# Optimization experiments

Hardware: AMD Instinct MI355X
Metric: run time of the kernel (lower is better)

Reference implementation:

```python
import jax, jax.numpy as jnp
import numpy as np


def setup_inputs() -> dict:
    key = jax.random.key(0)
    x = jax.random.normal(key, (4096, 4096), dtype=jnp.float32)
    return {"x": x}


def reference(x):
    """IDCT (DCT-III) along the last axis, scaled by 2 as in DREAMPlace:
        out[k] = x[0] + 2 * sum_{n=1}^{N-1} x[n] * cos(pi*n*(2k+1)/(2N))
    computed via a 2N-point FFT with twiddle-factor (expk) pre-multiply.
    """
    N = x.shape[-1]
    # twiddle expk[n] = exp(j*pi*n/(2N))
    theta = (jnp.pi / (2.0 * N)) * jnp.arange(N, dtype=jnp.float32)
    expk = jax.lax.complex(jnp.cos(theta), jnp.sin(theta))  # complex64 [N]
    c = x.astype(jnp.complex64) * expk                       # [M, N]
    # zero-pad to 2N; S[k] = sum_n c[n] exp(+j*2*pi*n*k/(2N)) = conj(fft(conj(c2)))[k]
    c2 = jnp.concatenate([c, jnp.zeros_like(c)], axis=-1)    # [M, 2N]
    S = jnp.fft.fft(jnp.conj(c2))                            # Re(S) == Re(2N*ifft(c2))
    # out[k] = 2*Re(S[k]) - x[0]
    y = 2.0 * jnp.real(S[..., :N]) - x[..., :1]
    return y.astype(x.dtype)
```

## Files before the change

kernel.cpp:

```cpp
#include <hip/hip_runtime.h>
#include <stdint.h>


#define Md 4096
#define Nfull 4096
#define Ph 2048
#define Kh 2048
#define BM 128
#define BN 128
#define BK 64

typedef short bf16x8 __attribute__((ext_vector_type(8)));
typedef float floatx4 __attribute__((ext_vector_type(4)));
typedef unsigned short ushort_t;

__device__ __forceinline__ ushort_t f2bf(float f) {
  union { float f; uint32_t u; } v; v.f = f;
  uint32_t u = v.u;
  return (ushort_t)((u + 0x7fffu + ((u >> 16) & 1u)) >> 16);
}

__global__ __launch_bounds__(256) void prep_kernel(const float* __restrict__ x,
                                                   ushort_t* __restrict__ A,
                                                   ushort_t* __restrict__ Ce,
                                                   ushort_t* __restrict__ Co) {
  int b = blockIdx.x;
  if (b < 8192) {
    int i = (b * 256 + threadIdx.x) * 8;
    int m = i >> 12;
    int j = i & 4095;
    float4 a = *(const float4*)(x + i);
    float4 c = *(const float4*)(x + i + 4);
    union { ushort_t us[4]; int2 v; } ev, od;
    ev.us[0] = f2bf(a.x); od.us[0] = f2bf(a.y);
    ev.us[1] = f2bf(a.z); od.us[1] = f2bf(a.w);
    ev.us[2] = f2bf(c.x); od.us[2] = f2bf(c.y);
    ev.us[3] = f2bf(c.z); od.us[3] = f2bf(c.w);
    int half = j >> 1;
    *(int2*)(A + m * Nfull + half) = ev.v;
    *(int2*)(A + m * Nfull + Ph + half) = od.v;
  } else {
    int idx = ((b - 8192) * 256 + threadIdx.x) * 8;
    const float s = 3.14159265358979f / 8192.0f;
    union { ushort_t us[8]; int4 v; } pk;
    if (idx < Ph * Kh) {
      int p = idx >> 11;
      int ne0 = idx & 2047;
      int tp = 2 * p + 1;
#pragma unroll
      for (int jj = 0; jj < 8; ++jj) {
        int n = 2 * (ne0 + jj);
        int t = (n * tp) & 16383;
        float c = (n == 0) ? 1.0f : 2.0f * __cosf(s * (float)t);
        pk.us[jj] = f2bf(c);
      }
      *(int4*)(Ce + idx) = pk.v;
    } else {
      int local = idx - Ph * Kh;
      int p = local >> 11;
      int no0 = local & 2047;
      int tp = 2 * p + 1;
#pragma unroll
      for (int jj = 0; jj < 8; ++jj) {
        int n = 2 * (no0 + jj) + 1;
        int t = (n * tp) & 16383;
        pk.us[jj] = f2bf(2.0f * __cosf(s * (float)t));
      }
      *(int4*)(Co + local) = pk.v;
    }
  }
}

__global__ __launch_bounds__(256, 2) void gemm_fused(const ushort_t* __restrict__ A,
                                                     const ushort_t* __restrict__ Ce,
                                                     const ushort_t* __restrict__ Co,
                                                     float* __restrict__ out) {
  __shared__ __align__(16) ushort_t AsE[BM * BK];
  __shared__ __align__(16) ushort_t AsO[BM * BK];
  __shared__ __align__(16) ushort_t BsE[BN * BK];
  __shared__ __align__(16) ushort_t BsO[BN * BK];

  const int tid = threadIdx.x;
  const int wid = tid >> 6;
  const int lane = tid & 63;

  const int bm = blockIdx.y * BM;
  const int bn = blockIdx.x * BN;

  const int wm = (wid & 1) * 64;
  const int wn = (wid >> 1) * 64;

  const int lrow = lane & 15;
  const int kq = (lane >> 4) * 8;

  floatx4 accE[4][4] = {};
  floatx4 accO[4][4] = {};

  const int rr = tid >> 3;
  const int ee = (tid & 7) * 8;
  const int lb = wid * 512;

  const ushort_t* Ae = A + (size_t)bm * Nfull;
  const ushort_t* Ao = Ae + Ph;
  const ushort_t* Be = Ce + (size_t)bn * Kh;
  const ushort_t* Bo = Co + (size_t)bn * Kh;

#define GLDS(src, dst) __builtin_amdgcn_global_load_lds( \
      (const __attribute__((address_space(1))) void*)(src), \
      (__attribute__((address_space(3))) void*)(dst), 16, 0, 0)

  for (int k0 = 0; k0 < Kh; k0 += BK) {
#pragma unroll
    for (int i = 0; i < 4; ++i) {
      int r = i * 32 + rr;
      int l = i * 2048 + lb;
      GLDS(Ae + (size_t)r * Nfull + k0 + ee, AsE + l);
      GLDS(Ao + (size_t)r * Nfull + k0 + ee, AsO + l);
      GLDS(Be + (size_t)r * Kh   + k0 + ee, BsE + l);
      GLDS(Bo + (size_t)r * Kh   + k0 + ee, BsO + l);
    }
    __syncthreads();

#pragma unroll
    for (int kk = 0; kk < 2; ++kk) {
      const int ko = kk * 32 + kq;
      bf16x8 bE[4], bO[4];
#pragma unroll
      for (int f = 0; f < 4; ++f) {
        bE[f] = *(const bf16x8*)(BsE + (wn + f * 16 + lrow) * BK + ko);
        bO[f] = *(const bf16x8*)(BsO + (wn + f * 16 + lrow) * BK + ko);
      }
#pragma unroll
      for (int im = 0; im < 4; ++im) {
        bf16x8 aE = *(const bf16x8*)(AsE + (wm + im * 16 + lrow) * BK + ko);
        bf16x8 aO = *(const bf16x8*)(AsO + (wm + im * 16 + lrow) * BK + ko);
#pragma unroll
        for (int jn = 0; jn < 4; ++jn) {
          accE[im][jn] = __builtin_amdgcn_mfma_f32_16x16x32_bf16(aE, bE[jn], accE[im][jn], 0, 0, 0);
          accO[im][jn] = __builtin_amdgcn_mfma_f32_16x16x32_bf16(aO, bO[jn], accO[im][jn], 0, 0, 0);
        }
      }
    }
    __syncthreads();
  }
#undef GLDS

#pragma unroll
  for (int im = 0; im < 4; ++im) {
    int rb = bm + wm + im * 16 + (lane >> 4) * 4;
#pragma unroll
    for (int jn = 0; jn < 4; ++jn) {
      int p = bn + wn + jn * 16 + lrow;
      float* lo = out + (size_t)rb * Nfull + p;
      float* hi = out + (size_t)rb * Nfull + (Nfull - 1 - p);
#pragma unroll
      for (int r = 0; r < 4; ++r) {
        float e = accE[im][jn][r];
        float o = accO[im][jn][r];
        lo[(size_t)r * Nfull] = e + o;
        hi[(size_t)r * Nfull] = e - o;
      }
    }
  }
}

extern "C" void kernel_launch(void* const* d_in, const int* in_sizes, int n_in,
                              void* d_out, int out_size, void* d_ws, size_t ws_size,
                              hipStream_t stream) {
  const float* x = (const float*)d_in[0];
  float* out = (float*)d_out;
  ushort_t* Axb = (ushort_t*)d_ws;
  ushort_t* Ce = Axb + (size_t)Md * Nfull;
  ushort_t* Co = Ce + (size_t)Ph * Kh;

  prep_kernel<<<12288, 256, 0, stream>>>(x, Axb, Ce, Co);

  dim3 grid(Ph / BN, Md / BM);
  gemm_fused<<<grid, 256, 0, stream>>>(Axb, Ce, Co, out);
}
```

Baseline: 195.2 us.

## Swizzle LDS tile layout to fragment-major order and widen prep conversion stores

The GEMM's global-to-LDS copy now places data so each 16-row by 32-k MFMA fragment is contiguous. Each lane reads its 16-byte operand at lane*8, which removes the strided row-major LDS reads and their bank conflicts. The prep kernel handles 16 floats per thread with 16-byte stores for the even and odd halves, halving its block count. The global load pattern changes to 16 rows by 32 columns per wave chunk, which may reduce global coalescing width per row.

```diff
diff --git a/kernel.cpp b/kernel.cpp
--- a/kernel.cpp
+++ b/kernel.cpp
@@ -25,22 +25,30 @@
                                                    ushort_t* __restrict__ Ce,
                                                    ushort_t* __restrict__ Co) {
   int b = blockIdx.x;
-  if (b < 8192) {
-    int i = (b * 256 + threadIdx.x) * 8;
+  int tid = threadIdx.x;
+  if (b < 4096) {
+    int i = (b * 256 + tid) * 16;
     int m = i >> 12;
     int j = i & 4095;
-    float4 a = *(const float4*)(x + i);
-    float4 c = *(const float4*)(x + i + 4);
-    union { ushort_t us[4]; int2 v; } ev, od;
-    ev.us[0] = f2bf(a.x); od.us[0] = f2bf(a.y);
-    ev.us[1] = f2bf(a.z); od.us[1] = f2bf(a.w);
-    ev.us[2] = f2bf(c.x); od.us[2] = f2bf(c.y);
-    ev.us[3] = f2bf(c.z); od.us[3] = f2bf(c.w);
+    const float4* xp = (const float4*)(x + i);
+    float4 a0 = xp[0];
+    float4 a1 = xp[1];
+    float4 a2 = xp[2];
+    float4 a3 = xp[3];
+    union { ushort_t us[8]; int4 v; } ev, od;
+    ev.us[0] = f2bf(a0.x); od.us[0] = f2bf(a0.y);
+    ev.us[1] = f2bf(a0.z); od.us[1] = f2bf(a0.w);
+    ev.us[2] = f2bf(a1.x); od.us[2] = f2bf(a1.y);
+    ev.us[3] = f2bf(a1.z); od.us[3] = f2bf(a1.w);
+    ev.us[4] = f2bf(a2.x); od.us[4] = f2bf(a2.y);
+    ev.us[5] = f2bf(a2.z); od.us[5] = f2bf(a2.w);
+    ev.us[6] = f2bf(a3.x); od.us[6] = f2bf(a3.y);
+    ev.us[7] = f2bf(a3.z); od.us[7] = f2bf(a3.w);
     int half = j >> 1;
-    *(int2*)(A + m * Nfull + half) = ev.v;
-    *(int2*)(A + m * Nfull + Ph + half) = od.v;
+    *(int4*)(A + (size_t)m * Nfull + half) = ev.v;
+    *(int4*)(A + (size_t)m * Nfull + Ph + half) = od.v;
   } else {
-    int idx = ((b - 8192) * 256 + threadIdx.x) * 8;
+    int idx = ((b - 4096) * 256 + tid) * 8;
     const float s = 3.14159265358979f / 8192.0f;
     union { ushort_t us[8]; int4 v; } pk;
     if (idx < Ph * Kh) {
@@ -91,19 +99,21 @@
   const int wn = (wid >> 1) * 64;
 
   const int lrow = lane & 15;
-  const int kq = (lane >> 4) * 8;
 
   floatx4 accE[4][4] = {};
   floatx4 accO[4][4] = {};
 
-  const int rr = tid >> 3;
-  const int ee = (tid & 7) * 8;
+  const int srow = ((tid >> 7) << 4) | (tid & 15);
+  const int scol = ((tid >> 6) & 1) * 32 + ((tid >> 4) & 3) * 8;
   const int lb = wid * 512;
 
   const ushort_t* Ae = A + (size_t)bm * Nfull;
   const ushort_t* Ao = Ae + Ph;
   const ushort_t* Be = Ce + (size_t)bn * Kh;
   const ushort_t* Bo = Co + (size_t)bn * Kh;
+
+  const size_t aoff0 = (size_t)srow * Nfull + scol;
+  const size_t boff0 = (size_t)srow * Kh + scol;
 
 #define GLDS(src, dst) __builtin_amdgcn_global_load_lds( \
       (const __attribute__((address_space(1))) void*)(src), \
@@ -112,28 +122,30 @@
   for (int k0 = 0; k0 < Kh; k0 += BK) {
 #pragma unroll
     for (int i = 0; i < 4; ++i) {
-      int r = i * 32 + rr;
+      size_t ao = aoff0 + (size_t)(i * 32) * Nfull + k0;
+      size_t bo = boff0 + (size_t)(i * 32) * Kh + k0;
       int l = i * 2048 + lb;
-      GLDS(Ae + (size_t)r * Nfull + k0 + ee, AsE + l);
-      GLDS(Ao + (size_t)r * Nfull + k0 + ee, AsO + l);
-      GLDS(Be + (size_t)r * Kh   + k0 + ee, BsE + l);
-      GLDS(Bo + (size_t)r * Kh   + k0 + ee, BsO + l);
+      GLDS(Ae + ao, AsE + l);
+      GLDS(Ao + ao, AsO + l);
+      GLDS(Be + bo, BsE + l);
+      GLDS(Bo + bo, BsO + l);
     }
     __syncthreads();
 
 #pragma unroll
     for (int kk = 0; kk < 2; ++kk) {
-      const int ko = kk * 32 + kq;
       bf16x8 bE[4], bO[4];
 #pragma unroll
       for (int f = 0; f < 4; ++f) {
-        bE[f] = *(const bf16x8*)(BsE + (wn + f * 16 + lrow) * BK + ko);
-        bO[f] = *(const bf16x8*)(BsO + (wn + f * 16 + lrow) * BK + ko);
+        int off = ((wn >> 4) + f) * 1024 + kk * 512 + lane * 8;
+        bE[f] = *(const bf16x8*)(BsE + off);
+        bO[f] = *(const bf16x8*)(BsO + off);
       }
 #pragma unroll
       for (int im = 0; im < 4; ++im) {
-        bf16x8 aE = *(const bf16x8*)(AsE + (wm + im * 16 + lrow) * BK + ko);
-        bf16x8 aO = *(const bf16x8*)(AsO + (wm + im * 16 + lrow) * BK + ko);
+        int off = ((wm >> 4) + im) * 1024 + kk * 512 + lane * 8;
+        bf16x8 aE = *(const bf16x8*)(AsE + off);
+        bf16x8 aO = *(const bf16x8*)(AsO + off);
 #pragma unroll
         for (int jn = 0; jn < 4; ++jn) {
           accE[im][jn] = __builtin_amdgcn_mfma_f32_16x16x32_bf16(aE, bE[jn], accE[im][jn], 0, 0, 0);
@@ -173,7 +185,7 @@
   ushort_t* Ce = Axb + (size_t)Md * Nfull;
   ushort_t* Co = Ce + (size_t)Ph * Kh;
 
-  prep_kernel<<<12288, 256, 0, stream>>>(x, Axb, Ce, Co);
+  prep_kernel<<<8192, 256, 0, stream>>>(x, Axb, Ce, Co);
 
   dim3 grid(Ph / BN, Md / BM);
   gemm_fused<<<grid, 256, 0, stream>>>(Axb, Ce, Co, out);
```

Measured after the change: 236.9 us. 1.21x slower.

## Pre-tile operands into K-block layout and double-buffer LDS in GEMM

Applied to the files above, without the earlier changes.

The prep kernel now writes the even/odd input planes and the cosine tables into a tiled layout: 128-row by 32-k blocks, each stored contiguously in a k-group-major order. The GEMM then loads each stage with fully contiguous global_load_lds transfers into a double-buffered LDS region, issuing the next stage's loads before computing the current one. This halves BK to 32 and drops one barrier per iteration, aiming to overlap global loads with MFMA work and to make LDS fragment reads conflict-free. The cost is twice as many K iterations and a larger LDS footprint, which may limit occupancy.

```diff
diff --git a/kernel.cpp b/kernel.cpp
--- a/kernel.cpp
+++ b/kernel.cpp
@@ -8,7 +8,9 @@
 #define Kh 2048
 #define BM 128
 #define BN 128
-#define BK 64
+#define BK 32
+#define NKB 64
+#define TILE 4096
 
 typedef short bf16x8 __attribute__((ext_vector_type(8)));
 typedef float floatx4 __attribute__((ext_vector_type(4)));
@@ -21,136 +23,153 @@
 }
 
 __global__ __launch_bounds__(256) void prep_kernel(const float* __restrict__ x,
-                                                   ushort_t* __restrict__ A,
+                                                   ushort_t* __restrict__ Ae,
+                                                   ushort_t* __restrict__ Ao,
                                                    ushort_t* __restrict__ Ce,
                                                    ushort_t* __restrict__ Co) {
   int b = blockIdx.x;
-  if (b < 8192) {
-    int i = (b * 256 + threadIdx.x) * 8;
-    int m = i >> 12;
-    int j = i & 4095;
-    float4 a = *(const float4*)(x + i);
-    float4 c = *(const float4*)(x + i + 4);
-    union { ushort_t us[4]; int2 v; } ev, od;
-    ev.us[0] = f2bf(a.x); od.us[0] = f2bf(a.y);
-    ev.us[1] = f2bf(a.z); od.us[1] = f2bf(a.w);
-    ev.us[2] = f2bf(c.x); od.us[2] = f2bf(c.y);
-    ev.us[3] = f2bf(c.z); od.us[3] = f2bf(c.w);
-    int half = j >> 1;
-    *(int2*)(A + m * Nfull + half) = ev.v;
-    *(int2*)(A + m * Nfull + Ph + half) = od.v;
+  int t = threadIdx.x;
+  if (b < 2048) {
+    int bm = b >> 6, kb = b & 63;
+    int r = t >> 1, h = t & 1;
+    const float4* xp = (const float4*)(x + (((size_t)(bm * 128 + r)) << 12) + kb * 64 + h * 32);
+    float4 v0 = xp[0], v1 = xp[1], v2 = xp[2], v3 = xp[3];
+    float4 v4 = xp[4], v5 = xp[5], v6 = xp[6], v7 = xp[7];
+    union { ushort_t us[8]; int4 v; } e0, e1, o0, o1;
+    e0.us[0] = f2bf(v0.x); o0.us[0] = f2bf(v0.y);
+    e0.us[1] = f2bf(v0.z); o0.us[1] = f2bf(v0.w);
+    e0.us[2] = f2bf(v1.x); o0.us[2] = f2bf(v1.y);
+    e0.us[3] = f2bf(v1.z); o0.us[3] = f2bf(v1.w);
+    e0.us[4] = f2bf(v2.x); o0.us[4] = f2bf(v2.y);
+    e0.us[5] = f2bf(v2.z); o0.us[5] = f2bf(v2.w);
+    e0.us[6] = f2bf(v3.x); o0.us[6] = f2bf(v3.y);
+    e0.us[7] = f2bf(v3.z); o0.us[7] = f2bf(v3.w);
+    e1.us[0] = f2bf(v4.x); o1.us[0] = f2bf(v4.y);
+    e1.us[1] = f2bf(v4.z); o1.us[1] = f2bf(v4.w);
+    e1.us[2] = f2bf(v5.x); o1.us[2] = f2bf(v5.y);
+    e1.us[3] = f2bf(v5.z); o1.us[3] = f2bf(v5.w);
+    e1.us[4] = f2bf(v6.x); o1.us[4] = f2bf(v6.y);
+    e1.us[5] = f2bf(v6.z); o1.us[5] = f2bf(v6.w);
+    e1.us[6] = f2bf(v7.x); o1.us[6] = f2bf(v7.y);
+    e1.us[7] = f2bf(v7.z); o1.us[7] = f2bf(v7.w);
+    size_t tb = ((size_t)(bm * 64 + kb)) << 12;
+    int c0 = (2 * h) * 1024 + r * 8;
+    int c1 = c0 + 1024;
+    *(int4*)(Ae + tb + c0) = e0.v;
+    *(int4*)(Ae + tb + c1) = e1.v;
+    *(int4*)(Ao + tb + c0) = o0.v;
+    *(int4*)(Ao + tb + c1) = o1.v;
   } else {
-    int idx = ((b - 8192) * 256 + threadIdx.x) * 8;
+    int b2 = b - 2048;
+    int plane = b2 >> 10;
+    int bn = (b2 & 1023) >> 6, kb = b2 & 63;
+    ushort_t* T = plane ? Co : Ce;
+    size_t tb = ((size_t)(bn * 64 + kb)) << 12;
     const float s = 3.14159265358979f / 8192.0f;
-    union { ushort_t us[8]; int4 v; } pk;
-    if (idx < Ph * Kh) {
-      int p = idx >> 11;
-      int ne0 = idx & 2047;
+#pragma unroll
+    for (int half = 0; half < 2; ++half) {
+      int cc = t + half * 256;
+      int g = cc >> 7, r = cc & 127;
+      int p = bn * 128 + r;
       int tp = 2 * p + 1;
+      int ni = kb * 32 + g * 8;
+      union { ushort_t us[8]; int4 v; } pk;
 #pragma unroll
       for (int jj = 0; jj < 8; ++jj) {
-        int n = 2 * (ne0 + jj);
-        int t = (n * tp) & 16383;
-        float c = (n == 0) ? 1.0f : 2.0f * __cosf(s * (float)t);
+        int n = 2 * (ni + jj) + plane;
+        int ang = (n * tp) & 16383;
+        float c = (n == 0) ? 1.0f : 2.0f * __cosf(s * (float)ang);
         pk.us[jj] = f2bf(c);
       }
-      *(int4*)(Ce + idx) = pk.v;
-    } else {
-      int local = idx - Ph * Kh;
-      int p = local >> 11;
-      int no0 = local & 2047;
-      int tp = 2 * p + 1;
-#pragma unroll
-      for (int jj = 0; jj < 8; ++jj) {
-        int n = 2 * (no0 + jj) + 1;
-        int t = (n * tp) & 16383;
-        pk.us[jj] = f2bf(2.0f * __cosf(s * (float)t));
-      }
-      *(int4*)(Co + local) = pk.v;
+      *(int4*)(T + tb + cc * 8) = pk.v;
     }
   }
 }
 
-__global__ __launch_bounds__(256, 2) void gemm_fused(const ushort_t* __restrict__ A,
+__global__ __launch_bounds__(256, 2) void gemm_fused(const ushort_t* __restrict__ Ae,
+                                                     const ushort_t* __restrict__ Ao,
                                                      const ushort_t* __restrict__ Ce,
                                                      const ushort_t* __restrict__ Co,
                                                      float* __restrict__ out) {
-  __shared__ __align__(16) ushort_t AsE[BM * BK];
-  __shared__ __align__(16) ushort_t AsO[BM * BK];
-  __shared__ __align__(16) ushort_t BsE[BN * BK];
-  __shared__ __align__(16) ushort_t BsO[BN * BK];
+  __shared__ __align__(16) ushort_t S[32768];
 
   const int tid = threadIdx.x;
   const int wid = tid >> 6;
   const int lane = tid & 63;
 
-  const int bm = blockIdx.y * BM;
-  const int bn = blockIdx.x * BN;
+  const int bm = blockIdx.y;
+  const int bn = blockIdx.x;
 
   const int wm = (wid & 1) * 64;
   const int wn = (wid >> 1) * 64;
-
   const int lrow = lane & 15;
-  const int kq = (lane >> 4) * 8;
 
   floatx4 accE[4][4] = {};
   floatx4 accO[4][4] = {};
 
-  const int rr = tid >> 3;
-  const int ee = (tid & 7) * 8;
   const int lb = wid * 512;
-
-  const ushort_t* Ae = A + (size_t)bm * Nfull;
-  const ushort_t* Ao = Ae + Ph;
-  const ushort_t* Be = Ce + (size_t)bn * Kh;
-  const ushort_t* Bo = Co + (size_t)bn * Kh;
+  const ushort_t* pAe = Ae + (((size_t)bm * NKB) << 12) + (tid << 3);
+  const ushort_t* pAo = Ao + (((size_t)bm * NKB) << 12) + (tid << 3);
+  const ushort_t* pBe = Ce + (((size_t)bn * NKB) << 12) + (tid << 3);
+  const ushort_t* pBo = Co + (((size_t)bn * NKB) << 12) + (tid << 3);
 
 #define GLDS(src, dst) __builtin_amdgcn_global_load_lds( \
       (const __attribute__((address_space(1))) void*)(src), \
       (__attribute__((address_space(3))) void*)(dst), 16, 0, 0)
 
-  for (int k0 = 0; k0 < Kh; k0 += BK) {
-#pragma unroll
-    for (int i = 0; i < 4; ++i) {
-      int r = i * 32 + rr;
-      int l = i * 2048 + lb;
-      GLDS(Ae + (size_t)r * Nfull + k0 + ee, AsE + l);
-      GLDS(Ao + (size_t)r * Nfull + k0 + ee, AsO + l);
-      GLDS(Be + (size_t)r * Kh   + k0 + ee, BsE + l);
-      GLDS(Bo + (size_t)r * Kh   + k0 + ee, BsO + l);
-    }
-    __syncthreads();
-
-#pragma unroll
-    for (int kk = 0; kk < 2; ++kk) {
-      const int ko = kk * 32 + kq;
-      bf16x8 bE[4], bO[4];
-#pragma unroll
-      for (int f = 0; f < 4; ++f) {
-        bE[f] = *(const bf16x8*)(BsE + (wn + f * 16 + lrow) * BK + ko);
-        bO[f] = *(const bf16x8*)(BsO + (wn + f * 16 + lrow) * BK + ko);
-      }
-#pragma unroll
-      for (int im = 0; im < 4; ++im) {
-        bf16x8 aE = *(const bf16x8*)(AsE + (wm + im * 16 + lrow) * BK + ko);
-        bf16x8 aO = *(const bf16x8*)(AsO + (wm + im * 16 + lrow) * BK + ko);
-#pragma unroll
-        for (int jn = 0; jn < 4; ++jn) {
-          accE[im][jn] = __builtin_amdgcn_mfma_f32_16x16x32_bf16(aE, bE[jn], accE[im][jn], 0, 0, 0);
-          accO[im][jn] = __builtin_amdgcn_mfma_f32_16x16x32_bf16(aO, bO[jn], accO[im][jn], 0, 0, 0);
-        }
-      }
-    }
+#define STAGE(bufoff, t) do { \
+    size_t so_ = ((size_t)(t)) << 12; \
+    _Pragma("unroll") \
+    for (int i_ = 0; i_ < 2; ++i_) { \
+      GLDS(pAe + so_ + i_ * 2048, S + (bufoff) + i_ * 2048 + lb); \
+      GLDS(pAo + so_ + i_ * 2048, S + (bufoff) + 4096 + i_ * 2048 + lb); \
+      GLDS(pBe + so_ + i_ * 2048, S + (bufoff) + 8192 + i_ * 2048 + lb); \
+      GLDS(pBo + so_ + i_ * 2048, S + (bufoff) + 12288 + i_ * 2048 + lb); \
+    } } while (0)
+
+  const int g1024 = (lane >> 4) << 10;
+  const int rb8 = lrow << 3;
+
+#define COMPUTE(bufoff) do { \
+    bf16x8 bE_[4], bO_[4]; \
+    _Pragma("unroll") \
+    for (int f_ = 0; f_ < 4; ++f_) { \
+      int off_ = (bufoff) + g1024 + rb8 + ((wn + f_ * 16) << 3); \
+      bE_[f_] = *(const bf16x8*)(S + 8192 + off_); \
+      bO_[f_] = *(const bf16x8*)(S + 12288 + off_); \
+    } \
+    _Pragma("unroll") \
+    for (int im_ = 0; im_ < 4; ++im_) { \
+      int off_ = (bufoff) + g1024 + rb8 + ((wm + im_ * 16) << 3); \
+      bf16x8 aE_ = *(const bf16x8*)(S + off_); \
+      bf16x8 aO_ = *(const bf16x8*)(S + 4096 + off_); \
+      _Pragma("unroll") \
+      for (int jn_ = 0; jn_ < 4; ++jn_) { \
+        accE[im_][jn_] = __builtin_amdgcn_mfma_f32_16x16x32_bf16(aE_, bE_[jn_], accE[im_][jn_], 0, 0, 0); \
+        accO[im_][jn_] = __builtin_amdgcn_mfma_f32_16x16x32_bf16(aO_, bO_[jn_], accO[im_][jn_], 0, 0, 0); \
+      } \
+    } } while (0)
+
+  STAGE(0, 0);
+  __syncthreads();
+  for (int t = 0; t < NKB - 1; ++t) {
+    const int cur = (t & 1) << 14;
+    STAGE(cur ^ 16384, t + 1);
+    COMPUTE(cur);
     __syncthreads();
   }
+  COMPUTE(16384);
+
 #undef GLDS
+#undef STAGE
+#undef COMPUTE
 
 #pragma unroll
   for (int im = 0; im < 4; ++im) {
-    int rb = bm + wm + im * 16 + (lane >> 4) * 4;
+    int rb = bm * BM + wm + im * 16 + (lane >> 4) * 4;
 #pragma unroll
     for (int jn = 0; jn < 4; ++jn) {
-      int p = bn + wn + jn * 16 + lrow;
+      int p = bn * BN + wn + jn * 16 + lrow;
       float* lo = out + (size_t)rb * Nfull + p;
       float* hi = out + (size_t)rb * Nfull + (Nfull - 1 - p);
 #pragma unroll
@@ -169,12 +188,13 @@
                               hipStream_t stream) {
   const float* x = (const float*)d_in[0];
   float* out = (float*)d_out;
-  ushort_t* Axb = (ushort_t*)d_ws;
-  ushort_t* Ce = Axb + (size_t)Md * Nfull;
-  ushort_t* Co = Ce + (size_t)Ph * Kh;
-
-  prep_kernel<<<12288, 256, 0, stream>>>(x, Axb, Ce, Co);
+  ushort_t* Ae = (ushort_t*)d_ws;
+  ushort_t* Ao = Ae + (size_t)8 * 1024 * 1024;
+  ushort_t* Ce = Ao + (size_t)8 * 1024 * 1024;
+  ushort_t* Co = Ce + (size_t)4 * 1024 * 1024;
+
+  prep_kernel<<<4096, 256, 0, stream>>>(x, Ae, Ao, Ce, Co);
 
   dim3 grid(Ph / BN, Md / BM);
-  gemm_fused<<<grid, 256, 0, stream>>>(Axb, Ce, Co, out);
-}
+  gemm_fused<<<grid, 256, 0, stream>>>(Ae, Ao, Ce, Co, out);
+}
```

After: 178.6 us. 8.5% less time.
